# Kernel optimization log

Hardware: AMD Instinct MI355X
Metric: run time of the kernel (lower is better)

Reference implementation:

```python
import jax, jax.numpy as jnp
import numpy as np

NOISE_STD = 0.5   # quantization_noise_std default in PSN.run
BETA = 0.25       # commitment-loss weight
B, E, C, K = 64, 256, 256, 8192


def setup_inputs() -> dict:
    key = jax.random.key(0)
    k1, k2, k3 = jax.random.split(key, 3)
    latents = jax.random.normal(k1, (B, E, C), dtype=jnp.float32)
    # initial_codebook: uniform(-1, 1) then mean-centered over the code axis
    codebook = jax.random.uniform(k2, (K, C), dtype=jnp.float32, minval=-1.0, maxval=1.0)
    codebook = codebook - codebook.mean(axis=0)
    noise = jax.random.normal(k3, (B * E, 1), dtype=jnp.float32)
    return {"latents": latents, "codebook": codebook, "noise": noise}


def reference(latents, codebook, noise):
    b, e, c = latents.shape
    k = codebook.shape[0]
    flat = latents.reshape(b * e, c)                      # (b s) (r c), r=1
    dist = (jnp.sum(flat * flat, axis=1, keepdims=True)
            + jnp.sum(codebook * codebook, axis=1)
            - 2.0 * jnp.matmul(flat, codebook.T))
    inds_det = jnp.argmin(dist, axis=1)                   # [N]
    offs = jnp.round(noise[:, 0] * NOISE_STD).astype(jnp.int32)
    inds_noisy = jnp.clip(inds_det.astype(jnp.int32) + offs, 0, k - 1)
    # one-hot @ codebook == gather (same math, same vjp scatter-add)
    q_det = codebook[inds_det].reshape(b, e, c)
    q_noisy = codebook[inds_noisy].reshape(b, e, c)
    # straight-through estimator output fed to the post-quantizer
    st = latents + jax.lax.stop_gradient(q_noisy - latents)
    # non_recon_loss(latents, q_det, q_noisy): beta*mse(latents, sg(q_det)) + mse(q_noisy, sg(latents))
    loss = (BETA * jnp.mean((latents - jax.lax.stop_gradient(q_det)) ** 2)
            + jnp.mean((q_noisy - jax.lax.stop_gradient(latents)) ** 2))
    return st, loss, inds_noisy.reshape(b, e)
```

## Files before the change

### kernel.cpp

```cpp
#include <hip/hip_runtime.h>
#include <hip/hip_bf16.h>


namespace {
constexpr int N_ROWS  = 16384;
constexpr int K_CODES = 8192;
constexpr int C_DIM   = 256;
constexpr float EPS_GAP = 0.004f;
}

typedef __attribute__((ext_vector_type(8)))  short bf16x8;
typedef __attribute__((ext_vector_type(16))) float f32x16;

typedef __attribute__((address_space(1))) const unsigned int gas_u32;
typedef __attribute__((address_space(3))) unsigned int las_u32;

__device__ __forceinline__ void gld16(const unsigned short* g, unsigned short* l) {
    __builtin_amdgcn_global_load_lds((gas_u32*)g, (las_u32*)l, 16, 0, 0);
}

__device__ __forceinline__ unsigned f2key(float f) {
    unsigned u = __float_as_uint(f);
    return (u & 0x80000000u) ? ~u : (u | 0x80000000u);
}
__device__ __forceinline__ float key2f(unsigned k) {
    unsigned u = (k & 0x80000000u) ? (k ^ 0x80000000u) : ~k;
    return __uint_as_float(u);
}
__device__ __forceinline__ unsigned short f2bf(float x) {
    unsigned u = __float_as_uint(x);
    unsigned r = u + 0x7fffu + ((u >> 16) & 1u);
    return (unsigned short)(r >> 16);
}

extern "C" __global__ void prep_kernel(const float* __restrict__ src,
                                       unsigned short* __restrict__ hi,
                                       unsigned short* __restrict__ lo) {
    const int i = (blockIdx.x * 256 + threadIdx.x) * 8;
    const int row = i >> 8, col = i & 255;
    const int d = (((row >> 5) * 8 + (col >> 5)) * 4 + ((col >> 3) & 3)) * 256
                + (row & 31) * 8;
    float4 a = *(const float4*)&src[i];
    float4 b = *(const float4*)&src[i + 4];
    float v[8] = {a.x, a.y, a.z, a.w, b.x, b.y, b.z, b.w};
    unsigned short h[8], l[8];
    #pragma unroll
    for (int j = 0; j < 8; ++j) {
        h[j] = f2bf(v[j]);
        float hf = __uint_as_float((unsigned)h[j] << 16);
        l[j] = f2bf(v[j] - hf);
    }
    ushort4 h0 = {h[0], h[1], h[2], h[3]}, h1 = {h[4], h[5], h[6], h[7]};
    ushort4 l0 = {l[0], l[1], l[2], l[3]}, l1 = {l[4], l[5], l[6], l[7]};
    *(ushort4*)&hi[d] = h0;  *(ushort4*)&hi[d + 4] = h1;
    *(ushort4*)&lo[d] = l0;  *(ushort4*)&lo[d + 4] = l1;
}

extern "C" __global__ void prepw_kernel(const float* __restrict__ src,
                                        unsigned short* __restrict__ hi,
                                        unsigned short* __restrict__ lo,
                                        float* __restrict__ wnorm) {
    const int i = (blockIdx.x * 256 + threadIdx.x) * 8;
    float4 a = *(const float4*)&src[i];
    float4 b = *(const float4*)&src[i + 4];
    float v[8] = {a.x, a.y, a.z, a.w, b.x, b.y, b.z, b.w};
    unsigned short h[8], l[8];
    float s = 0.0f;
    #pragma unroll
    for (int j = 0; j < 8; ++j) {
        h[j] = f2bf(v[j]);
        float hf = __uint_as_float((unsigned)h[j] << 16);
        l[j] = f2bf(v[j] - hf);
        s = fmaf(v[j], v[j], s);
    }
    ushort4 h0 = {h[0], h[1], h[2], h[3]}, h1 = {h[4], h[5], h[6], h[7]};
    ushort4 l0 = {l[0], l[1], l[2], l[3]}, l1 = {l[4], l[5], l[6], l[7]};
    *(ushort4*)&hi[i] = h0;  *(ushort4*)&hi[i + 4] = h1;
    *(ushort4*)&lo[i] = l0;  *(ushort4*)&lo[i + 4] = l1;
    #pragma unroll
    for (int m = 1; m < 32; m <<= 1) s += __shfl_xor(s, m, 64);
    if ((threadIdx.x & 31) == 0) wnorm[i >> 8] = s;
}

extern "C" __global__ void __launch_bounds__(256, 2)
pass1_kernel(const unsigned short* __restrict__ xh_g,
             const unsigned short* __restrict__ xl_g,
             const unsigned short* __restrict__ wh_g,
             const unsigned short* __restrict__ wl_g,
             const float* __restrict__ wnorm,
             unsigned long long* __restrict__ keys,
             unsigned* __restrict__ keys2) {
    __shared__ __align__(16) unsigned short LDS[2][2][128 * 32];
    const int tid = threadIdx.x;
    const int lane = tid & 63;
    const int wid = tid >> 6;
    const int wr = wid >> 1, wc = wid & 1;
    const int h = lane >> 5;
    const int l31 = lane & 31;
    const int rb = blockIdx.x & 127, cs = blockIdx.x >> 7;
    const int r0 = rb * 128, cbase = cs * 1024;

    const int dr = lane >> 2;
    const int gq = (lane & 3) ^ ((lane >> 3) & 3);
    const int laneoff = dr * 256 + gq * 8;

    const int rB0 = wc * 64 + l31, rB1 = rB0 + 32;
    const int fB = (rB0 >> 1) & 3;

    const size_t abase = ((size_t)(rb * 4 + wr * 2) * 8) * 1024 + h * 256 + l31 * 8;

    float bv[2][16];  unsigned bi[2][16];  float sv[2][16];
    #pragma unroll
    for (int tm = 0; tm < 2; ++tm)
        #pragma unroll
        for (int r = 0; r < 16; ++r) { bv[tm][r] = 3.4e38f; sv[tm][r] = 3.4e38f; bi[tm][r] = 0; }

    f32x16 acc[2][2];
    #pragma unroll
    for (int tm = 0; tm < 2; ++tm)
        #pragma unroll
        for (int tn = 0; tn < 2; ++tn)
            #pragma unroll
            for (int e = 0; e < 16; ++e) acc[tm][tn][e] = 0.0f;

    auto stageW = [&](int t, int b) {
        const int kc32 = (t & 7) * 32;
        const int cb = cbase + (t >> 3) * 128;
        #pragma unroll
        for (int c = 0; c < 2; ++c) {
            const int R = wid * 32 + c * 16;
            const size_t wg = (size_t)(cb + R) * 256 + kc32 + laneoff;
            gld16(wh_g + wg, &LDS[b][0][R * 32]);
            gld16(wl_g + wg, &LDS[b][1][R * 32]);
        }
    };

#define LOADA(Ph00, Ph01, Ph10, Ph11, Pl00, Pl01, Pl10, Pl11, tt)              \
    {   const size_t o_ = abase + (size_t)((tt) & 7) * 1024;                   \
        Ph00 = *(const bf16x8*)(xh_g + o_);                                    \
        Ph01 = *(const bf16x8*)(xh_g + o_ + 512);                              \
        Ph10 = *(const bf16x8*)(xh_g + o_ + 8192);                             \
        Ph11 = *(const bf16x8*)(xh_g + o_ + 8704);                             \
        Pl00 = *(const bf16x8*)(xl_g + o_);                                    \
        Pl01 = *(const bf16x8*)(xl_g + o_ + 512);                              \
        Pl10 = *(const bf16x8*)(xl_g + o_ + 8192);                             \
        Pl11 = *(const bf16x8*)(xl_g + o_ + 8704);                             \
    }

#define MFMA_TILE(Ph00, Ph01, Ph10, Ph11, Pl00, Pl01, Pl10, Pl11, P)           \
    {   _Pragma("unroll")                                                      \
        for (int kk = 0; kk < 2; ++kk) {                                       \
            const int q = kk * 2 + h;                                          \
            const int aB0 = rB0 * 32 + ((q ^ fB) << 3);                        \
            const int aB1 = rB1 * 32 + ((q ^ fB) << 3);                        \
            bf16x8 b0h = *(const bf16x8*)&LDS[P][0][aB0];                      \
            bf16x8 b1h = *(const bf16x8*)&LDS[P][0][aB1];                      \
            bf16x8 b0l = *(const bf16x8*)&LDS[P][1][aB0];                      \
            bf16x8 b1l = *(const bf16x8*)&LDS[P][1][aB1];                      \
            bf16x8 a0h = kk ? Ph01 : Ph00;                                     \
            bf16x8 a1h = kk ? Ph11 : Ph10;                                     \
            bf16x8 a0l = kk ? Pl01 : Pl00;                                     \
            bf16x8 a1l = kk ? Pl11 : Pl10;                                     \
            acc[0][0] = __builtin_amdgcn_mfma_f32_32x32x16_bf16(a0h, b0h, acc[0][0], 0, 0, 0); \
            acc[0][1] = __builtin_amdgcn_mfma_f32_32x32x16_bf16(a0h, b1h, acc[0][1], 0, 0, 0); \
            acc[1][0] = __builtin_amdgcn_mfma_f32_32x32x16_bf16(a1h, b0h, acc[1][0], 0, 0, 0); \
            acc[1][1] = __builtin_amdgcn_mfma_f32_32x32x16_bf16(a1h, b1h, acc[1][1], 0, 0, 0); \
            acc[0][0] = __builtin_amdgcn_mfma_f32_32x32x16_bf16(a0h, b0l, acc[0][0], 0, 0, 0); \
            acc[0][1] = __builtin_amdgcn_mfma_f32_32x32x16_bf16(a0h, b1l, acc[0][1], 0, 0, 0); \
            acc[1][0] = __builtin_amdgcn_mfma_f32_32x32x16_bf16(a1h, b0l, acc[1][0], 0, 0, 0); \
            acc[1][1] = __builtin_amdgcn_mfma_f32_32x32x16_bf16(a1h, b1l, acc[1][1], 0, 0, 0); \
            acc[0][0] = __builtin_amdgcn_mfma_f32_32x32x16_bf16(a0l, b0h, acc[0][0], 0, 0, 0); \
            acc[0][1] = __builtin_amdgcn_mfma_f32_32x32x16_bf16(a0l, b1h, acc[0][1], 0, 0, 0); \
            acc[1][0] = __builtin_amdgcn_mfma_f32_32x32x16_bf16(a1l, b0h, acc[1][0], 0, 0, 0); \
            acc[1][1] = __builtin_amdgcn_mfma_f32_32x32x16_bf16(a1l, b1h, acc[1][1], 0, 0, 0); \
        }                                                                      \
    }

    auto epilogue = [&](int t) {
        const int cb = cbase + (t >> 3) * 128;
        const float wnA = wnorm[cb + wc * 64 + l31];
        const float wnB = wnorm[cb + wc * 64 + 32 + l31];
        const unsigned cA = cb + wc * 64 + l31;
        const unsigned cB = cA + 32;
        #pragma unroll
        for (int tm = 0; tm < 2; ++tm)
            #pragma unroll
            for (int r = 0; r < 16; ++r) {
                float s0 = fmaf(-2.0f, acc[tm][0][r], wnA);
                bool c0 = s0 < bv[tm][r];
                sv[tm][r] = fminf(sv[tm][r], c0 ? bv[tm][r] : s0);
                bv[tm][r] = c0 ? s0 : bv[tm][r];
                bi[tm][r] = c0 ? cA : bi[tm][r];
                float s1 = fmaf(-2.0f, acc[tm][1][r], wnB);
                bool c1 = s1 < bv[tm][r];
                sv[tm][r] = fminf(sv[tm][r], c1 ? bv[tm][r] : s1);
                bv[tm][r] = c1 ? s1 : bv[tm][r];
                bi[tm][r] = c1 ? cB : bi[tm][r];
            }
        #pragma unroll
        for (int tm = 0; tm < 2; ++tm)
            #pragma unroll
            for (int tn = 0; tn < 2; ++tn)
                #pragma unroll
                for (int e = 0; e < 16; ++e) acc[tm][tn][e] = 0.0f;
    };

    bf16x8 cAh00, cAh01, cAh10, cAh11, cAl00, cAl01, cAl10, cAl11;
    bf16x8 nAh00, nAh01, nAh10, nAh11, nAl00, nAl01, nAl10, nAl11;

    LOADA(cAh00, cAh01, cAh10, cAh11, cAl00, cAl01, cAl10, cAl11, 0);
    stageW(0, 0);
    __syncthreads();

    for (int t2 = 0; t2 < 64; t2 += 2) {
        stageW(t2 + 1, 1);
        LOADA(nAh00, nAh01, nAh10, nAh11, nAl00, nAl01, nAl10, nAl11, t2 + 1);
        MFMA_TILE(cAh00, cAh01, cAh10, cAh11, cAl00, cAl01, cAl10, cAl11, 0);
        __syncthreads();

        if (t2 + 2 < 64) {
            stageW(t2 + 2, 0);
            LOADA(cAh00, cAh01, cAh10, cAh11, cAl00, cAl01, cAl10, cAl11, t2 + 2);
        }
        MFMA_TILE(nAh00, nAh01, nAh10, nAh11, nAl00, nAl01, nAl10, nAl11, 1);
        if (((t2 + 1) & 7) == 7) epilogue(t2 + 1);
        __syncthreads();
    }
#undef LOADA
#undef MFMA_TILE

    #pragma unroll
    for (int tm = 0; tm < 2; ++tm)
        #pragma unroll
        for (int r = 0; r < 16; ++r) {
            unsigned long long key =
                ((unsigned long long)f2key(bv[tm][r]) << 32) | bi[tm][r];
            unsigned sk = f2key(sv[tm][r]);
            #pragma unroll
            for (int m = 1; m < 32; m <<= 1) {
                unsigned long long ko = __shfl_xor(key, m, 64);
                unsigned sko = __shfl_xor(sk, m, 64);
                unsigned long long loser = key < ko ? ko : key;
                sk = min(min(sk, sko), (unsigned)(loser >> 32));
                key = key < ko ? key : ko;
            }
            if (l31 == 0) {
                const int grow = r0 + wr * 64 + tm * 32 + (r & 3) + 8 * (r >> 2) + 4 * h;
                unsigned long long old = atomicMin(&keys[grow], key);
                if (old != ~0ull) {
                    unsigned long long loser = old < key ? key : old;
                    atomicMin(&keys2[grow], (unsigned)(loser >> 32));
                }
                atomicMin(&keys2[grow], sk);
            }
        }
}

extern "C" __global__ void flag_kernel(unsigned long long* __restrict__ keys,
                                       const unsigned* __restrict__ keys2,
                                       int* __restrict__ list, int* __restrict__ count) {
    const int row = blockIdx.x * 256 + threadIdx.x;
    unsigned long long k = keys[row];
    float b = key2f((unsigned)(k >> 32));
    float s = key2f(keys2[row]);
    if (s - b < EPS_GAP) {
        int p = atomicAdd(count, 1);
        list[p] = row;
        keys[row] = ~0ull;
    }
}

extern "C" __global__ void __launch_bounds__(256)
rerank_kernel(const float* __restrict__ lat,
              const float* __restrict__ cbk,
              const float* __restrict__ wnorm,
              const int* __restrict__ list,
              const int* __restrict__ count,
              unsigned long long* __restrict__ keys) {
    const int w = threadIdx.x >> 6, lane = threadIdx.x & 63;
    const int c0 = blockIdx.x * 16 + w * 4;
    float4 wv0 = *(const float4*)&cbk[(size_t)(c0 + 0) * C_DIM + lane * 4];
    float4 wv1 = *(const float4*)&cbk[(size_t)(c0 + 1) * C_DIM + lane * 4];
    float4 wv2 = *(const float4*)&cbk[(size_t)(c0 + 2) * C_DIM + lane * 4];
    float4 wv3 = *(const float4*)&cbk[(size_t)(c0 + 3) * C_DIM + lane * 4];
    const float wn0 = wnorm[c0 + 0], wn1 = wnorm[c0 + 1];
    const float wn2 = wnorm[c0 + 2], wn3 = wnorm[c0 + 3];
    const int n = *count;

    auto dot4 = [&](const float4& x, const float4& v) {
        float d = x.x * v.x;
        d = fmaf(x.y, v.y, d);
        d = fmaf(x.z, v.z, d);
        return fmaf(x.w, v.w, d);
    };
    auto best4 = [&](float a0, float a1, float a2, float a3) {
        unsigned long long k0 = ((unsigned long long)f2key(fmaf(-2.0f, a0, wn0)) << 32) | (unsigned)(c0 + 0);
        unsigned long long k1 = ((unsigned long long)f2key(fmaf(-2.0f, a1, wn1)) << 32) | (unsigned)(c0 + 1);
        unsigned long long k2 = ((unsigned long long)f2key(fmaf(-2.0f, a2, wn2)) << 32) | (unsigned)(c0 + 2);
        unsigned long long k3 = ((unsigned long long)f2key(fmaf(-2.0f, a3, wn3)) << 32) | (unsigned)(c0 + 3);
        unsigned long long b01 = k0 < k1 ? k0 : k1;
        unsigned long long b23 = k2 < k3 ? k2 : k3;
        return b01 < b23 ? b01 : b23;
    };

    int i = 0;
    for (; i + 2 <= n; i += 2) {
        const int r0 = list[i], r1 = list[i + 1];
        float4 x0 = *(const float4*)&lat[(size_t)r0 * C_DIM + lane * 4];
        float4 x1 = *(const float4*)&lat[(size_t)r1 * C_DIM + lane * 4];
        float d00 = dot4(x0, wv0), d01 = dot4(x0, wv1), d02 = dot4(x0, wv2), d03 = dot4(x0, wv3);
        float d10 = dot4(x1, wv0), d11 = dot4(x1, wv1), d12 = dot4(x1, wv2), d13 = dot4(x1, wv3);
        #pragma unroll
        for (int m = 1; m < 64; m <<= 1) {
            d00 += __shfl_xor(d00, m, 64); d01 += __shfl_xor(d01, m, 64);
            d02 += __shfl_xor(d02, m, 64); d03 += __shfl_xor(d03, m, 64);
            d10 += __shfl_xor(d10, m, 64); d11 += __shfl_xor(d11, m, 64);
            d12 += __shfl_xor(d12, m, 64); d13 += __shfl_xor(d13, m, 64);
        }
        if (lane == 0) {
            unsigned long long b0 = best4(d00, d01, d02, d03);
            unsigned long long b1 = best4(d10, d11, d12, d13);
            if (b0 < keys[r0]) atomicMin(&keys[r0], b0);
            if (b1 < keys[r1]) atomicMin(&keys[r1], b1);
        }
    }
    if (i < n) {
        const int r0 = list[i];
        float4 x0 = *(const float4*)&lat[(size_t)r0 * C_DIM + lane * 4];
        float d00 = dot4(x0, wv0), d01 = dot4(x0, wv1), d02 = dot4(x0, wv2), d03 = dot4(x0, wv3);
        #pragma unroll
        for (int m = 1; m < 64; m <<= 1) {
            d00 += __shfl_xor(d00, m, 64); d01 += __shfl_xor(d01, m, 64);
            d02 += __shfl_xor(d02, m, 64); d03 += __shfl_xor(d03, m, 64);
        }
        if (lane == 0) {
            unsigned long long b0 = best4(d00, d01, d02, d03);
            if (b0 < keys[r0]) atomicMin(&keys[r0], b0);
        }
    }
}

extern "C" __global__ void finalize_kernel(const float* __restrict__ lat,
                                           const float* __restrict__ cbk,
                                           const float* __restrict__ noise,
                                           const unsigned long long* __restrict__ keys,
                                           float* __restrict__ out,
                                           float* __restrict__ lpart) {
    const int g = threadIdx.x >> 5;
    const int l = threadIdx.x & 31;
    const int row = blockIdx.x * 8 + g;
    const unsigned long long p = keys[row];
    const int id = (int)(unsigned)(p & 0xFFFFFFFFull);
    const int off = (int)rintf(noise[row] * 0.5f);
    int idn = id + off;
    idn = idn < 0 ? 0 : (idn > K_CODES - 1 ? K_CODES - 1 : idn);
    const float4* latp = (const float4*)&lat[(size_t)row * C_DIM];
    const float4* qdp  = (const float4*)&cbk[(size_t)id  * C_DIM];
    const float4* qnp  = (const float4*)&cbk[(size_t)idn * C_DIM];
    float4* stp = (float4*)&out[(size_t)row * C_DIM];
    float t = 0.0f;
    #pragma unroll
    for (int j = 0; j < 2; ++j) {
        const int e = l + j * 32;
        float4 x  = latp[e];
        float4 qd = qdp[e];
        float4 qn = qnp[e];
        float4 st = {x.x + (qn.x - x.x), x.y + (qn.y - x.y),
                     x.z + (qn.z - x.z), x.w + (qn.w - x.w)};
        stp[e] = st;
        float d1, d2;
        d1 = x.x - qd.x; d2 = qn.x - x.x; t += 0.25f * d1 * d1 + d2 * d2;
        d1 = x.y - qd.y; d2 = qn.y - x.y; t += 0.25f * d1 * d1 + d2 * d2;
        d1 = x.z - qd.z; d2 = qn.z - x.z; t += 0.25f * d1 * d1 + d2 * d2;
        d1 = x.w - qd.w; d2 = qn.w - x.w; t += 0.25f * d1 * d1 + d2 * d2;
    }
    t *= (1.0f / 4194304.0f);
    #pragma unroll
    for (int m = 1; m < 32; m <<= 1) t += __shfl_xor(t, m, 64);
    __shared__ float red[8];
    if (l == 0) {
        red[g] = t;
        out[(size_t)N_ROWS * C_DIM + 1 + row] = (float)idn;
    }
    __syncthreads();
    if (threadIdx.x == 0) {
        float s = red[0] + red[1] + red[2] + red[3] + red[4] + red[5] + red[6] + red[7];
        atomicAdd(&lpart[blockIdx.x & 1023], s);
    }
}

extern "C" __global__ void loss_reduce_kernel(const float* __restrict__ lpart,
                                              float* __restrict__ out) {
    const int t = threadIdx.x;
    float s = lpart[t] + lpart[t + 256] + lpart[t + 512] + lpart[t + 768];
    #pragma unroll
    for (int m = 32; m; m >>= 1) s += __shfl_xor(s, m, 64);
    __shared__ float red[4];
    if ((t & 63) == 0) red[t >> 6] = s;
    __syncthreads();
    if (t == 0) out[(size_t)N_ROWS * C_DIM] = red[0] + red[1] + red[2] + red[3];
}

extern "C" void kernel_launch(void* const* d_in, const int* in_sizes, int n_in,
                              void* d_out, int out_size, void* d_ws, size_t ws_size,
                              hipStream_t stream) {
    const float* lat   = (const float*)d_in[0];
    const float* cbk   = (const float*)d_in[1];
    const float* noise = (const float*)d_in[2];
    float* out = (float*)d_out;

    char* ws = (char*)d_ws;
    unsigned short* xh = (unsigned short*)(ws);
    unsigned short* xl = (unsigned short*)(ws + 8388608);
    unsigned short* wh = (unsigned short*)(ws + 16777216);
    unsigned short* wl = (unsigned short*)(ws + 20971520);
    float* wnorm       = (float*)(ws + 25165824);
    unsigned long long* keys = (unsigned long long*)(ws + 25198592);
    unsigned* keys2    = (unsigned*)(ws + 25329664);
    int* list          = (int*)(ws + 25395200);
    float* lpart       = (float*)(ws + 25460736);
    int* count         = (int*)(ws + 25464832);

    hipMemsetAsync(keys, 0xFF, 192 * 1024, stream);
    hipMemsetAsync(lpart, 0, 4096 + 4, stream);

    prep_kernel <<<2048, 256, 0, stream>>>(lat, xh, xl);
    prepw_kernel<<<1024, 256, 0, stream>>>(cbk, wh, wl, wnorm);
    pass1_kernel<<<1024, 256, 0, stream>>>(xh, xl, wh, wl, wnorm, keys, keys2);
    flag_kernel <<<N_ROWS / 256, 256, 0, stream>>>(keys, keys2, list, count);
    rerank_kernel<<<512, 256, 0, stream>>>(lat, cbk, wnorm, list, count, keys);
    finalize_kernel<<<N_ROWS / 8, 256, 0, stream>>>(lat, cbk, noise, keys, out, lpart);
    loss_reduce_kernel<<<1, 256, 0, stream>>>(lpart, out);
}
```

Measured before the change: 303.0 us.

## Stage 64-wide K chunks of codebook per barrier and remap block order

The codebook staging tile is widened from 32 to 64 K-columns per stage, so each double-buffered LDS stage covers two MFMA chunks. This halves the number of __syncthreads per tile (32 stages instead of 64 steps with two barriers each). The LDS swizzle is changed to an 8-way XOR pattern to match the wider rows. Block indexing is also reordered so the 8 codebook slices of one row block are adjacent, which changes L2 reuse of the latent rows. LDS use doubles to 64 KB per block, which could limit occupancy under the 2-blocks-per-CU launch bound.

Result: slower. 339.1 us (+11.9%).

```diff
diff --git a/kernel.cpp b/kernel.cpp
--- a/kernel.cpp
+++ b/kernel.cpp
@@ -90,22 +90,20 @@
              const float* __restrict__ wnorm,
              unsigned long long* __restrict__ keys,
              unsigned* __restrict__ keys2) {
-    __shared__ __align__(16) unsigned short LDS[2][2][128 * 32];
+    __shared__ __align__(16) unsigned short LDS[2][2][128 * 64];
     const int tid = threadIdx.x;
     const int lane = tid & 63;
     const int wid = tid >> 6;
     const int wr = wid >> 1, wc = wid & 1;
     const int h = lane >> 5;
     const int l31 = lane & 31;
-    const int rb = blockIdx.x & 127, cs = blockIdx.x >> 7;
+    const int rb = blockIdx.x >> 3, cs = blockIdx.x & 7;
     const int r0 = rb * 128, cbase = cs * 1024;
 
-    const int dr = lane >> 2;
-    const int gq = (lane & 3) ^ ((lane >> 3) & 3);
-    const int laneoff = dr * 256 + gq * 8;
+    const int laneoffW = (lane >> 3) * 256 + (((lane & 7) ^ (lane >> 3)) << 3);
 
     const int rB0 = wc * 64 + l31, rB1 = rB0 + 32;
-    const int fB = (rB0 >> 1) & 3;
+    const int fB = l31 & 7;
 
     const size_t abase = ((size_t)(rb * 4 + wr * 2) * 8) * 1024 + h * 256 + l31 * 8;
 
@@ -123,44 +121,44 @@
             #pragma unroll
             for (int e = 0; e < 16; ++e) acc[tm][tn][e] = 0.0f;
 
-    auto stageW = [&](int t, int b) {
-        const int kc32 = (t & 7) * 32;
-        const int cb = cbase + (t >> 3) * 128;
-        #pragma unroll
-        for (int c = 0; c < 2; ++c) {
-            const int R = wid * 32 + c * 16;
-            const size_t wg = (size_t)(cb + R) * 256 + kc32 + laneoff;
-            gld16(wh_g + wg, &LDS[b][0][R * 32]);
-            gld16(wl_g + wg, &LDS[b][1][R * 32]);
+    auto stageW = [&](int s, int b) {
+        const int kc = (s & 3) * 64;
+        const int cb = cbase + (s >> 2) * 128;
+        #pragma unroll
+        for (int c8 = 0; c8 < 4; ++c8) {
+            const int R = wid * 32 + c8 * 8;
+            const size_t wg = (size_t)(cb + R) * 256 + kc + laneoffW;
+            gld16(wh_g + wg, &LDS[b][0][R * 64]);
+            gld16(wl_g + wg, &LDS[b][1][R * 64]);
         }
     };
 
-#define LOADA(Ph00, Ph01, Ph10, Ph11, Pl00, Pl01, Pl10, Pl11, tt)              \
-    {   const size_t o_ = abase + (size_t)((tt) & 7) * 1024;                   \
-        Ph00 = *(const bf16x8*)(xh_g + o_);                                    \
-        Ph01 = *(const bf16x8*)(xh_g + o_ + 512);                              \
-        Ph10 = *(const bf16x8*)(xh_g + o_ + 8192);                             \
-        Ph11 = *(const bf16x8*)(xh_g + o_ + 8704);                             \
-        Pl00 = *(const bf16x8*)(xl_g + o_);                                    \
-        Pl01 = *(const bf16x8*)(xl_g + o_ + 512);                              \
-        Pl10 = *(const bf16x8*)(xl_g + o_ + 8192);                             \
-        Pl11 = *(const bf16x8*)(xl_g + o_ + 8704);                             \
-    }
-
-#define MFMA_TILE(Ph00, Ph01, Ph10, Ph11, Pl00, Pl01, Pl10, Pl11, P)           \
-    {   _Pragma("unroll")                                                      \
-        for (int kk = 0; kk < 2; ++kk) {                                       \
-            const int q = kk * 2 + h;                                          \
-            const int aB0 = rB0 * 32 + ((q ^ fB) << 3);                        \
-            const int aB1 = rB1 * 32 + ((q ^ fB) << 3);                        \
-            bf16x8 b0h = *(const bf16x8*)&LDS[P][0][aB0];                      \
-            bf16x8 b1h = *(const bf16x8*)&LDS[P][0][aB1];                      \
-            bf16x8 b0l = *(const bf16x8*)&LDS[P][1][aB0];                      \
-            bf16x8 b1l = *(const bf16x8*)&LDS[P][1][aB1];                      \
-            bf16x8 a0h = kk ? Ph01 : Ph00;                                     \
-            bf16x8 a1h = kk ? Ph11 : Ph10;                                     \
-            bf16x8 a0l = kk ? Pl01 : Pl00;                                     \
-            bf16x8 a1l = kk ? Pl11 : Pl10;                                     \
+#define LOADA(Ph00, Ph01, Ph10, Ph11, Pl00, Pl01, Pl10, Pl11, cc)             \
+    {   const size_t o_ = abase + (size_t)((cc) & 7) * 1024;                  \
+        Ph00 = *(const bf16x8*)(xh_g + o_);                                   \
+        Ph01 = *(const bf16x8*)(xh_g + o_ + 512);                             \
+        Ph10 = *(const bf16x8*)(xh_g + o_ + 8192);                            \
+        Ph11 = *(const bf16x8*)(xh_g + o_ + 8704);                            \
+        Pl00 = *(const bf16x8*)(xl_g + o_);                                   \
+        Pl01 = *(const bf16x8*)(xl_g + o_ + 512);                             \
+        Pl10 = *(const bf16x8*)(xl_g + o_ + 8192);                            \
+        Pl11 = *(const bf16x8*)(xl_g + o_ + 8704);                            \
+    }
+
+#define MFMA_CHUNK(Ph00, Ph01, Ph10, Ph11, Pl00, Pl01, Pl10, Pl11, P, J)      \
+    {   _Pragma("unroll")                                                     \
+        for (int kk = 0; kk < 2; ++kk) {                                      \
+            const int q8 = (J) * 4 + kk * 2 + h;                              \
+            const int aB0 = rB0 * 64 + ((q8 ^ fB) << 3);                      \
+            const int aB1 = rB1 * 64 + ((q8 ^ fB) << 3);                      \
+            bf16x8 b0h = *(const bf16x8*)&LDS[P][0][aB0];                     \
+            bf16x8 b1h = *(const bf16x8*)&LDS[P][0][aB1];                     \
+            bf16x8 b0l = *(const bf16x8*)&LDS[P][1][aB0];                     \
+            bf16x8 b1l = *(const bf16x8*)&LDS[P][1][aB1];                     \
+            bf16x8 a0h = kk ? Ph01 : Ph00;                                    \
+            bf16x8 a1h = kk ? Ph11 : Ph10;                                    \
+            bf16x8 a0l = kk ? Pl01 : Pl00;                                    \
+            bf16x8 a1l = kk ? Pl11 : Pl10;                                    \
             acc[0][0] = __builtin_amdgcn_mfma_f32_32x32x16_bf16(a0h, b0h, acc[0][0], 0, 0, 0); \
             acc[0][1] = __builtin_amdgcn_mfma_f32_32x32x16_bf16(a0h, b1h, acc[0][1], 0, 0, 0); \
             acc[1][0] = __builtin_amdgcn_mfma_f32_32x32x16_bf16(a1h, b0h, acc[1][0], 0, 0, 0); \
@@ -173,11 +171,11 @@
             acc[0][1] = __builtin_amdgcn_mfma_f32_32x32x16_bf16(a0l, b1h, acc[0][1], 0, 0, 0); \
             acc[1][0] = __builtin_amdgcn_mfma_f32_32x32x16_bf16(a1l, b0h, acc[1][0], 0, 0, 0); \
             acc[1][1] = __builtin_amdgcn_mfma_f32_32x32x16_bf16(a1l, b1h, acc[1][1], 0, 0, 0); \
-        }                                                                      \
-    }
-
-    auto epilogue = [&](int t) {
-        const int cb = cbase + (t >> 3) * 128;
+        }                                                                     \
+    }
+
+    auto epilogue = [&](int s) {
+        const int cb = cbase + (s >> 2) * 128;
         const float wnA = wnorm[cb + wc * 64 + l31];
         const float wnB = wnorm[cb + wc * 64 + 32 + l31];
         const unsigned cA = cb + wc * 64 + l31;
@@ -211,23 +209,19 @@
     LOADA(cAh00, cAh01, cAh10, cAh11, cAl00, cAl01, cAl10, cAl11, 0);
     stageW(0, 0);
     __syncthreads();
-
-    for (int t2 = 0; t2 < 64; t2 += 2) {
-        stageW(t2 + 1, 1);
-        LOADA(nAh00, nAh01, nAh10, nAh11, nAl00, nAl01, nAl10, nAl11, t2 + 1);
-        MFMA_TILE(cAh00, cAh01, cAh10, cAh11, cAl00, cAl01, cAl10, cAl11, 0);
+    int p = 0;
+    for (int s = 0; s < 32; ++s) {
+        if (s < 31) stageW(s + 1, p ^ 1);
+        LOADA(nAh00, nAh01, nAh10, nAh11, nAl00, nAl01, nAl10, nAl11, 2 * s + 1);
+        MFMA_CHUNK(cAh00, cAh01, cAh10, cAh11, cAl00, cAl01, cAl10, cAl11, p, 0);
+        if (s < 31) LOADA(cAh00, cAh01, cAh10, cAh11, cAl00, cAl01, cAl10, cAl11, 2 * s + 2);
+        MFMA_CHUNK(nAh00, nAh01, nAh10, nAh11, nAl00, nAl01, nAl10, nAl11, p, 1);
+        if ((s & 3) == 3) epilogue(s);
         __syncthreads();
-
-        if (t2 + 2 < 64) {
-            stageW(t2 + 2, 0);
-            LOADA(cAh00, cAh01, cAh10, cAh11, cAl00, cAl01, cAl10, cAl11, t2 + 2);
-        }
-        MFMA_TILE(nAh00, nAh01, nAh10, nAh11, nAl00, nAl01, nAl10, nAl11, 1);
-        if (((t2 + 1) & 7) == 7) epilogue(t2 + 1);
-        __syncthreads();
+        p ^= 1;
     }
 #undef LOADA
-#undef MFMA_TILE
+#undef MFMA_CHUNK
 
     #pragma unroll
     for (int tm = 0; tm < 2; ++tm)
```

## Drop A-register double buffering and raise occupancy to three blocks per SM

Applied to the files above, without the earlier changes.

Removes the second set of A-fragment registers that prefetched the next tile's latents from global memory. Each iteration now loads A for the current tile and uses it immediately, which frees VGPRs. The launch bound is raised to three blocks per CU so that more resident waves can hide that exposed global-load latency. The trade-off is that the MFMA chain now stalls on the A loads within each wave, and the compiler may spill registers under the tighter budget.

Measured after the change: 512.7 us. 69.2% more time.

```diff
diff --git a/kernel.cpp b/kernel.cpp
--- a/kernel.cpp
+++ b/kernel.cpp
@@ -82,7 +82,7 @@
     if ((threadIdx.x & 31) == 0) wnorm[i >> 8] = s;
 }
 
-extern "C" __global__ void __launch_bounds__(256, 2)
+extern "C" __global__ void __launch_bounds__(256, 3)
 pass1_kernel(const unsigned short* __restrict__ xh_g,
              const unsigned short* __restrict__ xl_g,
              const unsigned short* __restrict__ wh_g,
@@ -135,19 +135,21 @@
         }
     };
 
-#define LOADA(Ph00, Ph01, Ph10, Ph11, Pl00, Pl01, Pl10, Pl11, tt)              \
+    bf16x8 Ah00, Ah01, Ah10, Ah11, Al00, Al01, Al10, Al11;
+
+#define LOADA(tt)                                                              \
     {   const size_t o_ = abase + (size_t)((tt) & 7) * 1024;                   \
-        Ph00 = *(const bf16x8*)(xh_g + o_);                                    \
-        Ph01 = *(const bf16x8*)(xh_g + o_ + 512);                              \
-        Ph10 = *(const bf16x8*)(xh_g + o_ + 8192);                             \
-        Ph11 = *(const bf16x8*)(xh_g + o_ + 8704);                             \
-        Pl00 = *(const bf16x8*)(xl_g + o_);                                    \
-        Pl01 = *(const bf16x8*)(xl_g + o_ + 512);                              \
-        Pl10 = *(const bf16x8*)(xl_g + o_ + 8192);                             \
-        Pl11 = *(const bf16x8*)(xl_g + o_ + 8704);                             \
-    }
-
-#define MFMA_TILE(Ph00, Ph01, Ph10, Ph11, Pl00, Pl01, Pl10, Pl11, P)           \
+        Ah00 = *(const bf16x8*)(xh_g + o_);                                    \
+        Ah01 = *(const bf16x8*)(xh_g + o_ + 512);                              \
+        Ah10 = *(const bf16x8*)(xh_g + o_ + 8192);                             \
+        Ah11 = *(const bf16x8*)(xh_g + o_ + 8704);                             \
+        Al00 = *(const bf16x8*)(xl_g + o_);                                    \
+        Al01 = *(const bf16x8*)(xl_g + o_ + 512);                              \
+        Al10 = *(const bf16x8*)(xl_g + o_ + 8192);                             \
+        Al11 = *(const bf16x8*)(xl_g + o_ + 8704);                             \
+    }
+
+#define MFMA_TILE(P)                                                           \
     {   _Pragma("unroll")                                                      \
         for (int kk = 0; kk < 2; ++kk) {                                       \
             const int q = kk * 2 + h;                                          \
@@ -157,10 +159,10 @@
             bf16x8 b1h = *(const bf16x8*)&LDS[P][0][aB1];                      \
             bf16x8 b0l = *(const bf16x8*)&LDS[P][1][aB0];                      \
             bf16x8 b1l = *(const bf16x8*)&LDS[P][1][aB1];                      \
-            bf16x8 a0h = kk ? Ph01 : Ph00;                                     \
-            bf16x8 a1h = kk ? Ph11 : Ph10;                                     \
-            bf16x8 a0l = kk ? Pl01 : Pl00;                                     \
-            bf16x8 a1l = kk ? Pl11 : Pl10;                                     \
+            bf16x8 a0h = kk ? Ah01 : Ah00;                                     \
+            bf16x8 a1h = kk ? Ah11 : Ah10;                                     \
+            bf16x8 a0l = kk ? Al01 : Al00;                                     \
+            bf16x8 a1l = kk ? Al11 : Al10;                                     \
             acc[0][0] = __builtin_amdgcn_mfma_f32_32x32x16_bf16(a0h, b0h, acc[0][0], 0, 0, 0); \
             acc[0][1] = __builtin_amdgcn_mfma_f32_32x32x16_bf16(a0h, b1h, acc[0][1], 0, 0, 0); \
             acc[1][0] = __builtin_amdgcn_mfma_f32_32x32x16_bf16(a1h, b0h, acc[1][0], 0, 0, 0); \
@@ -205,26 +207,16 @@
                 for (int e = 0; e < 16; ++e) acc[tm][tn][e] = 0.0f;
     };
 
-    bf16x8 cAh00, cAh01, cAh10, cAh11, cAl00, cAl01, cAl10, cAl11;
-    bf16x8 nAh00, nAh01, nAh10, nAh11, nAl00, nAl01, nAl10, nAl11;
-
-    LOADA(cAh00, cAh01, cAh10, cAh11, cAl00, cAl01, cAl10, cAl11, 0);
     stageW(0, 0);
     __syncthreads();
-
-    for (int t2 = 0; t2 < 64; t2 += 2) {
-        stageW(t2 + 1, 1);
-        LOADA(nAh00, nAh01, nAh10, nAh11, nAl00, nAl01, nAl10, nAl11, t2 + 1);
-        MFMA_TILE(cAh00, cAh01, cAh10, cAh11, cAl00, cAl01, cAl10, cAl11, 0);
+    int p = 0;
+    for (int t = 0; t < 64; ++t) {
+        if (t < 63) stageW(t + 1, p ^ 1);
+        LOADA(t);
+        MFMA_TILE(p);
+        if ((t & 7) == 7) epilogue(t);
         __syncthreads();
-
-        if (t2 + 2 < 64) {
-            stageW(t2 + 2, 0);
-            LOADA(cAh00, cAh01, cAh10, cAh11, cAl00, cAl01, cAl10, cAl11, t2 + 2);
-        }
-        MFMA_TILE(nAh00, nAh01, nAh10, nAh11, nAl00, nAl01, nAl10, nAl11, 1);
-        if (((t2 + 1) & 7) == 7) epilogue(t2 + 1);
-        __syncthreads();
+        p ^= 1;
     }
 #undef LOADA
 #undef MFMA_TILE
```
